# Kernel tuning notes

Measured on AMD Instinct MI355X. Metric: run time of the kernel, lower is better.

Reference implementation:

```python
import jax, jax.numpy as jnp
import numpy as np

EPS = 1e-5  # BatchNorm eps; BN applied in eval mode with running_mean=0, running_var=1


def conv1x1(x, w, b=None):
    # x: [B,C,H,W], w: [O,C] -> [B,O,H,W]
    y = jnp.einsum('bchw,oc->bohw', x, w)
    if b is not None:
        y = y + b[None, :, None, None]
    return y


def bn_eval(x, gamma, beta):
    # running_mean=0, running_var=1
    scale = gamma / jnp.sqrt(1.0 + EPS)
    return x * scale[None, :, None, None] + beta[None, :, None, None]


def glnl_forward(x, mask, wt_nl, bt_nl, wp_nl, bp_nl, wt_l, bt_l, wp_l, bp_l,
                 wg_nl, bg_nl, wg_l, bg_l, wW, bW, gW, betaW, wWl, gWl, betaWl):
    B, C, H, W = x.shape
    I = wt_nl.shape[0]
    N = H * W

    # non-local branch score [B,N,N]
    th_nl = conv1x1(x, wt_nl, bt_nl).reshape(B, I, N)
    ph_nl = conv1x1(x, wp_nl, bp_nl).reshape(B, I, N)
    score_nl = jax.nn.softmax(jnp.einsum('bin,bim->bnm', th_nl, ph_nl), axis=-1)

    # local branch: mask-gated projections, score [B,N,N]
    m = mask.reshape(B, 1, N)
    th_l = conv1x1(x, wt_l, bt_l).reshape(B, I, N) * m
    ph_l = conv1x1(x, wp_l, bp_l).reshape(B, I, N) * m
    score_l = jax.nn.softmax(jnp.einsum('bin,bim->bnm', th_l, ph_l), axis=-1)

    # value projections [B,I,N]
    g_nl = conv1x1(x, wg_nl, bg_nl).reshape(B, I, N)
    g_l = conv1x1(x, wg_l, bg_l).reshape(B, I, N)

    # attention aggregation -> [B,I,H,W]
    y_nl = jnp.einsum('bnm,bim->bin', score_nl, g_nl).reshape(B, I, H, W)
    y_l = jnp.einsum('bnm,bim->bin', score_l, g_l).reshape(B, I, H, W)

    # W_local: conv1x1 (no bias) -> ReLU -> BN
    y_l = bn_eval(jax.nn.relu(conv1x1(y_l, wWl)), gWl, betaWl)

    y = y_nl + y_l
    # W: conv1x1 -> ReLU -> BN, then residual
    W_y = bn_eval(jax.nn.relu(conv1x1(y, wW, bW)), gW, betaW)
    return W_y + x


def setup_inputs() -> dict:
    key = jax.random.key(0)
    ks = jax.random.split(key, 20)
    B, C, I, H, W = 4, 128, 64, 64, 64
    s = 0.02
    inp = {
        'x': jax.random.normal(ks[0], (B, C, H, W), jnp.float32),
        'mask': (jax.random.uniform(ks[1], (B, 1, H, W)) > 0.5).astype(jnp.float32),
        'wt_nl': jax.random.normal(ks[2], (I, C)) * s, 'bt_nl': jnp.zeros((I,)),
        'wp_nl': jax.random.normal(ks[3], (I, C)) * s, 'bp_nl': jnp.zeros((I,)),
        'wt_l': jax.random.normal(ks[4], (I, C)) * s, 'bt_l': jnp.zeros((I,)),
        'wp_l': jax.random.normal(ks[5], (I, C)) * s, 'bp_l': jnp.zeros((I,)),
        'wg_nl': jax.random.normal(ks[6], (I, C)) * s, 'bg_nl': jnp.zeros((I,)),
        'wg_l': jax.random.normal(ks[7], (I, C)) * s, 'bg_l': jnp.zeros((I,)),
        'wW': jax.random.normal(ks[8], (C, I)) * s, 'bW': jnp.zeros((C,)),
        'gW': jnp.ones((C,)), 'betaW': jnp.zeros((C,)),
        'wWl': jax.random.normal(ks[9], (I, I)) * s,
        'gWl': jnp.ones((I,)), 'betaWl': jnp.zeros((I,)),
    }
    return inp


def reference(x, mask, wt_nl, bt_nl, wp_nl, bp_nl, wt_l, bt_l, wp_l, bp_l,
              wg_nl, bg_nl, wg_l, bg_l, wW, bW, gW, betaW, wWl, gWl, betaWl):
    return glnl_forward(x, mask, wt_nl, bt_nl, wp_nl, bp_nl, wt_l, bt_l, wp_l, bp_l,
                        wg_nl, bg_nl, wg_l, bg_l, wW, bW, gW, betaW, wWl, gWl, betaWl)
```

## Files before the change

### kernel.cpp

```cpp
#include <hip/hip_runtime.h>

typedef unsigned short u16;
typedef __attribute__((ext_vector_type(8))) short short8;
typedef __attribute__((ext_vector_type(4))) float floatx4;

#define MFMA16(a, b, c) __builtin_amdgcn_mfma_f32_16x16x32_bf16((a), (b), (c), 0, 0, 0)

#define SZ_P ((size_t)4 * 64 * 4096)
#define SZ_X ((size_t)4 * 128 * 4096)

__device__ __forceinline__ float bf2f(u16 u) {
    union { unsigned int i; float f; } v; v.i = ((unsigned int)u) << 16; return v.f;
}
__device__ __forceinline__ u16 f2bf(float f) {
    union { float f; unsigned int i; } v; v.f = f;
    unsigned int r = v.i + 0x7fffu + ((v.i >> 16) & 1u);
    return (u16)(r >> 16);
}
__device__ __forceinline__ unsigned int pk2(float a, float b) {
    union { float f; unsigned int u; } x, y; x.f = a; y.f = b;
    return (x.u >> 16) | (y.u & 0xffff0000u);
}

__global__ __launch_bounds__(256) void k_prep_x(const float* __restrict__ x,
                                                u16* __restrict__ xT) {
    __shared__ u16 tile[64][65];
    const int n0 = blockIdx.x * 64, c0 = blockIdx.y * 64, b = blockIdx.z;
    const int t = threadIdx.x;
    for (int idx = t; idx < 4096; idx += 256) {
        const int c = idx >> 6, n = idx & 63;
        tile[c][n] = f2bf(x[((size_t)b << 19) + ((size_t)(c0 + c) << 12) + n0 + n]);
    }
    __syncthreads();
    for (int idx = t; idx < 4096; idx += 256) {
        const int n = idx >> 6, c = idx & 63;
        xT[((size_t)b << 19) + (size_t)(n0 + n) * 128 + c0 + c] = tile[c][n];
    }
}

__global__ __launch_bounds__(256) void k_prep_w(
    const float* __restrict__ w0, const float* __restrict__ w1,
    const float* __restrict__ w2, const float* __restrict__ w3,
    const float* __restrict__ w4, const float* __restrict__ w5,
    const float* __restrict__ wWl, const float* __restrict__ wW,
    u16* __restrict__ wbf)
{
    const int idx = blockIdx.x * 256 + threadIdx.x;
    float v;
    if (idx < 49152) {
        const int j = idx >> 13, off = idx & 8191;
        const float* s = (j == 0) ? w0 : (j == 1) ? w1 : (j == 2) ? w2
                       : (j == 3) ? w3 : (j == 4) ? w4 : w5;
        v = s[off];
    } else if (idx < 53248) {
        v = wWl[idx - 49152];
    } else {
        v = wW[idx - 53248];
    }
    wbf[idx] = f2bf(v);
}

__global__ __launch_bounds__(256) void k_proj(
    const u16* __restrict__ xT, const float* __restrict__ mask,
    const u16* __restrict__ wbf,
    const float* __restrict__ bq0f, const float* __restrict__ bk0f,
    const float* __restrict__ bv0f,
    const float* __restrict__ bq1f, const float* __restrict__ bk1f,
    const float* __restrict__ bv1f,
    u16* __restrict__ q0, u16* __restrict__ k0, u16* __restrict__ v0,
    u16* __restrict__ q1, u16* __restrict__ k1, u16* __restrict__ v1)
{
    const int n0 = blockIdx.x * 64, b = blockIdx.y, br = blockIdx.z;
    const u16* wq = wbf + br * 24576;
    const u16* wk = wq + 8192;
    const u16* wv = wk + 8192;
    const float* bq = br ? bq1f : bq0f;
    const float* bk = br ? bk1f : bk0f;
    const float* bv = br ? bv1f : bv0f;
    u16* q = br ? q1 : q0;  u16* k = br ? k1 : k0;  u16* v = br ? v1 : v0;

    const int t = threadIdx.x, w = t >> 6, lane = t & 63;
    const int quad = lane >> 4, l15 = lane & 15;
    const u16* xb = xT + ((size_t)b << 19) + (size_t)n0 * 128;

    short8 ax[4];
#pragma unroll
    for (int cc = 0; cc < 4; ++cc)
        ax[cc] = *(const short8*)(xb + (w * 16 + l15) * 128 + quad * 8 + cc * 32);

    float mv[4] = {1.f, 1.f, 1.f, 1.f};
    if (br) {
#pragma unroll
        for (int r = 0; r < 4; ++r)
            mv[r] = mask[((size_t)b << 12) + n0 + w * 16 + quad * 4 + r];
    }

#pragma unroll
    for (int qk = 0; qk < 2; ++qk) {
        const u16* wsel = qk ? wk : wq;
        const float* bb = qk ? bk : bq;
        u16* o = qk ? k : q;
#pragma unroll
        for (int ns = 0; ns < 4; ++ns) {
            floatx4 acc = {0.f, 0.f, 0.f, 0.f};
            const u16* wp = wsel + (ns * 16 + l15) * 128 + quad * 8;
#pragma unroll
            for (int cc = 0; cc < 4; ++cc)
                acc = MFMA16(ax[cc], *(const short8*)(wp + cc * 32), acc);
            const float bias_i = bb[ns * 16 + l15];
#pragma unroll
            for (int r = 0; r < 4; ++r) {
                const float val = (acc[r] + bias_i) * mv[r];
                o[((size_t)b << 18) + (size_t)(n0 + w * 16 + quad * 4 + r) * 64
                  + ns * 16 + l15] = f2bf(val);
            }
        }
    }

    short8 aw[4];
#pragma unroll
    for (int cc = 0; cc < 4; ++cc)
        aw[cc] = *(const short8*)(wv + (w * 16 + l15) * 128 + quad * 8 + cc * 32);
    float bvr[4];
#pragma unroll
    for (int r = 0; r < 4; ++r) bvr[r] = bv[w * 16 + quad * 4 + r];
#pragma unroll
    for (int ns = 0; ns < 4; ++ns) {
        floatx4 acc = {0.f, 0.f, 0.f, 0.f};
#pragma unroll
        for (int cc = 0; cc < 4; ++cc)
            acc = MFMA16(aw[cc],
                *(const short8*)(xb + (ns * 16 + l15) * 128 + quad * 8 + cc * 32), acc);
#pragma unroll
        for (int r = 0; r < 4; ++r) {
            v[((size_t)b << 18) + ((size_t)(w * 16 + quad * 4 + r) << 12)
              + n0 + ns * 16 + l15] = f2bf(acc[r] + bvr[r]);
        }
    }
}

__global__ __launch_bounds__(256) void k_flash(
    const u16* __restrict__ Q0, const u16* __restrict__ K0,
    const u16* __restrict__ V0,
    const u16* __restrict__ Q1, const u16* __restrict__ K1,
    const u16* __restrict__ V1,
    u16* __restrict__ num, float* __restrict__ den)
{
    __shared__ __align__(16) u16 kt_s[2][64 * 72];
    __shared__ __align__(16) u16 vt_s[2][64 * 72];
    __shared__ __align__(16) u16 p_s[4 * 32 * 72];

    const int flat = blockIdx.x;
    const int g = flat & 15, tile = flat >> 4;
    const int b = g >> 2, z = g & 3;
    const int br = z >> 1, sp = z & 1;
    const int qb = tile * 128;
    const size_t base = ((size_t)b << 18);
    const u16* Q = (br ? Q1 : Q0) + base;
    const u16* K = (br ? K1 : K0) + base;
    const u16* V = (br ? V1 : V0) + base;
    u16* numo = num + (size_t)z * SZ_P + base;
    float* deno = den + z * 16384 + b * 4096;

    const int t = threadIdx.x, w = t >> 6, lane = t & 63;
    const int quad = lane >> 4, l15 = lane & 15;
    const int pw = w * 32 * 72;

    short8 aq[2][2];
#pragma unroll
    for (int t2 = 0; t2 < 2; ++t2)
#pragma unroll
        for (int s = 0; s < 2; ++s)
            aq[t2][s] = *(const short8*)(Q + (size_t)(qb + w * 32 + t2 * 16 + l15) * 64
                                         + s * 32 + quad * 8);

    floatx4 oacc[4][2];
#pragma unroll
    for (int it = 0; it < 4; ++it)
#pragma unroll
        for (int t2 = 0; t2 < 2; ++t2) oacc[it][t2] = (floatx4){0.f, 0.f, 0.f, 0.f};
    float dacc[2] = {0.f, 0.f};

    const int roff = tile & 31;
    const int m_beg = sp * 2048;

    {
        const int m0 = m_beg + (roff << 6);
#pragma unroll
        for (int u = 0; u < 2; ++u) {
            const int ch = t + u * 256, row = ch >> 3, cg = ch & 7;
            *(short8*)&kt_s[0][row * 72 + cg * 8] =
                *(const short8*)(K + (size_t)(m0 + row) * 64 + cg * 8);
            *(short8*)&vt_s[0][row * 72 + cg * 8] =
                *(const short8*)(V + ((size_t)row << 12) + m0 + cg * 8);
        }
    }

    for (int j = 0; j < 32; ++j) {
        const int cur = j & 1;
        const int mn = m_beg + (((roff + j + 1) & 31) << 6);
        short8 pkr[2], pvr[2];
#pragma unroll
        for (int u = 0; u < 2; ++u) {
            const int ch = t + u * 256, row = ch >> 3, cg = ch & 7;
            pkr[u] = *(const short8*)(K + (size_t)(mn + row) * 64 + cg * 8);
            pvr[u] = *(const short8*)(V + ((size_t)row << 12) + mn + cg * 8);
        }
        __syncthreads();

#pragma unroll
        for (int mt = 0; mt < 4; ++mt) {
            const u16* kp = &kt_s[cur][(mt * 16 + l15) * 72 + quad * 8];
            const short8 ka0 = *(const short8*)kp;
            const short8 ka1 = *(const short8*)(kp + 32);
#pragma unroll
            for (int t2 = 0; t2 < 2; ++t2) {
                floatx4 acc = {0.f, 0.f, 0.f, 0.f};
                acc = MFMA16(ka0, aq[t2][0], acc);
                acc = MFMA16(ka1, aq[t2][1], acc);
                const float e0 = __expf(acc[0]), e1 = __expf(acc[1]);
                const float e2 = __expf(acc[2]), e3 = __expf(acc[3]);
                dacc[t2] += (e0 + e1) + (e2 + e3);
                *(uint2*)&p_s[pw + (t2 * 16 + l15) * 72 + mt * 16 + quad * 4] =
                    make_uint2(pk2(e0, e1), pk2(e2, e3));
            }
        }

        short8 pb2[2][2];
#pragma unroll
        for (int t2 = 0; t2 < 2; ++t2)
#pragma unroll
            for (int s = 0; s < 2; ++s)
                pb2[t2][s] = *(const short8*)&p_s[pw + (t2 * 16 + l15) * 72 + s * 32 + quad * 8];
#pragma unroll
        for (int it = 0; it < 4; ++it) {
            const u16* vp = &vt_s[cur][(it * 16 + l15) * 72 + quad * 8];
            const short8 va0 = *(const short8*)vp;
            const short8 va1 = *(const short8*)(vp + 32);
#pragma unroll
            for (int t2 = 0; t2 < 2; ++t2) {
                oacc[it][t2] = MFMA16(va0, pb2[t2][0], oacc[it][t2]);
                oacc[it][t2] = MFMA16(va1, pb2[t2][1], oacc[it][t2]);
            }
        }

#pragma unroll
        for (int u = 0; u < 2; ++u) {
            const int ch = t + u * 256, row = ch >> 3, cg = ch & 7;
            *(short8*)&kt_s[cur ^ 1][row * 72 + cg * 8] = pkr[u];
            *(short8*)&vt_s[cur ^ 1][row * 72 + cg * 8] = pvr[u];
        }
    }

#pragma unroll
    for (int t2 = 0; t2 < 2; ++t2) {
        float d = dacc[t2];
        d += __shfl_xor(d, 16, 64);
        d += __shfl_xor(d, 32, 64);
        if (quad == 0) deno[qb + w * 32 + t2 * 16 + l15] = d;
    }

#pragma unroll
    for (int it = 0; it < 4; ++it)
#pragma unroll
        for (int t2 = 0; t2 < 2; ++t2) {
            *(uint2*)&p_s[pw + (t2 * 16 + l15) * 72 + it * 16 + quad * 4] =
                make_uint2(pk2(oacc[it][t2][0], oacc[it][t2][1]),
                           pk2(oacc[it][t2][2], oacc[it][t2][3]));
        }
    __syncthreads();
#pragma unroll
    for (int ch = t; ch < 1024; ch += 256) {
        const int row = ch >> 3, cg = ch & 7;
        *(short8*)(numo + (size_t)(qb + row) * 64 + cg * 8) =
            *(const short8*)&p_s[(row >> 5) * 2304 + (row & 31) * 72 + cg * 8];
    }
}

__global__ __launch_bounds__(256) void k_epi(
    const u16* __restrict__ num, const float* __restrict__ den,
    const u16* __restrict__ wbf,
    const float* __restrict__ gWl, const float* __restrict__ betaWl,
    const float* __restrict__ bW, const float* __restrict__ gW,
    const float* __restrict__ betaW,
    const float* __restrict__ x, float* __restrict__ out)
{
    __shared__ __align__(16) u16 yl_s[32 * 72];
    __shared__ __align__(16) u16 ynl_s[32 * 72];
    __shared__ __align__(16) u16 yy_s[32 * 72];
    const int b = blockIdx.y, n0 = blockIdx.x * 32, rb = blockIdx.z;
    const int t = threadIdx.x, w = t >> 6, lane = t & 63;
    const int quad = lane >> 4, l15 = lane & 15;
    const size_t ybase = ((size_t)b << 18) + (size_t)n0 * 64;

    {
        const int row = t >> 3, cg = t & 7;
        const float dn = den[b * 4096 + n0 + row] + den[16384 + b * 4096 + n0 + row];
        const float dl = den[32768 + b * 4096 + n0 + row] + den[49152 + b * 4096 + n0 + row];
        const float inl = 1.0f / dn, ilo = 1.0f / dl;
        const short8 a0 = *(const short8*)(num + ybase + row * 64 + cg * 8);
        const short8 a1 = *(const short8*)(num + SZ_P + ybase + row * 64 + cg * 8);
        const short8 c0 = *(const short8*)(num + 2 * SZ_P + ybase + row * 64 + cg * 8);
        const short8 c1 = *(const short8*)(num + 3 * SZ_P + ybase + row * 64 + cg * 8);
        short8 ynl8, yl8;
#pragma unroll
        for (int j = 0; j < 8; ++j) {
            ynl8[j] = (short)f2bf((bf2f((u16)a0[j]) + bf2f((u16)a1[j])) * inl);
            yl8[j]  = (short)f2bf((bf2f((u16)c0[j]) + bf2f((u16)c1[j])) * ilo);
        }
        *(short8*)&ynl_s[row * 72 + cg * 8] = ynl8;
        *(short8*)&yl_s[row * 72 + cg * 8] = yl8;
    }
    __syncthreads();
    const float rsq = rsqrtf(1.0f + 1e-5f);
    const u16* wblW = wbf + 49152;
    const u16* wbW  = wbf + 53248;

    {
        const short8 a0 = *(const short8*)(wblW + (w * 16 + l15) * 64 + quad * 8);
        const short8 a1 = *(const short8*)(wblW + (w * 16 + l15) * 64 + 32 + quad * 8);
        float sc[4], bt[4];
#pragma unroll
        for (int r = 0; r < 4; ++r) {
            const int io = w * 16 + quad * 4 + r;
            sc[r] = gWl[io] * rsq;
            bt[r] = betaWl[io];
        }
#pragma unroll
        for (int ns = 0; ns < 2; ++ns) {
            floatx4 acc = {0.f, 0.f, 0.f, 0.f};
            const u16* bp_ = &yl_s[(ns * 16 + l15) * 72 + quad * 8];
            acc = MFMA16(a0, *(const short8*)bp_, acc);
            acc = MFMA16(a1, *(const short8*)(bp_ + 32), acc);
#pragma unroll
            for (int r = 0; r < 4; ++r) {
                const int io = w * 16 + quad * 4 + r;
                float val = fmaxf(acc[r], 0.f) * sc[r] + bt[r];
                val += bf2f(ynl_s[(ns * 16 + l15) * 72 + io]);
                yy_s[(ns * 16 + l15) * 72 + io] = f2bf(val);
            }
        }
    }
    __syncthreads();

    {
        const int c0 = rb * 64 + w * 16;
        const short8 a0 = *(const short8*)(wbW + (c0 + l15) * 64 + quad * 8);
        const short8 a1 = *(const short8*)(wbW + (c0 + l15) * 64 + 32 + quad * 8);
        float bs[4], sc[4], bt[4];
#pragma unroll
        for (int r = 0; r < 4; ++r) {
            const int c = c0 + quad * 4 + r;
            bs[r] = bW[c];
            sc[r] = gW[c] * rsq;
            bt[r] = betaW[c];
        }
#pragma unroll
        for (int ns = 0; ns < 2; ++ns) {
            floatx4 acc = {0.f, 0.f, 0.f, 0.f};
            const u16* bp_ = &yy_s[(ns * 16 + l15) * 72 + quad * 8];
            acc = MFMA16(a0, *(const short8*)bp_, acc);
            acc = MFMA16(a1, *(const short8*)(bp_ + 32), acc);
#pragma unroll
            for (int r = 0; r < 4; ++r) {
                const int c = c0 + quad * 4 + r;
                float val = fmaxf(acc[r] + bs[r], 0.f) * sc[r] + bt[r];
                const size_t xi = ((size_t)b << 19) + ((size_t)c << 12) + n0 + ns * 16 + l15;
                out[xi] = val + x[xi];
            }
        }
    }
}

extern "C" void kernel_launch(void* const* d_in, const int* in_sizes, int n_in,
                              void* d_out, int out_size, void* d_ws, size_t ws_size,
                              hipStream_t stream) {
    const float* x      = (const float*)d_in[0];
    const float* mask   = (const float*)d_in[1];
    const float* wt_nl  = (const float*)d_in[2];  const float* bt_nl = (const float*)d_in[3];
    const float* wp_nl  = (const float*)d_in[4];  const float* bp_nl = (const float*)d_in[5];
    const float* wt_l   = (const float*)d_in[6];  const float* bt_l  = (const float*)d_in[7];
    const float* wp_l   = (const float*)d_in[8];  const float* bp_l  = (const float*)d_in[9];
    const float* wg_nl  = (const float*)d_in[10]; const float* bg_nl = (const float*)d_in[11];
    const float* wg_l   = (const float*)d_in[12]; const float* bg_l  = (const float*)d_in[13];
    const float* wW     = (const float*)d_in[14]; const float* bW    = (const float*)d_in[15];
    const float* gW     = (const float*)d_in[16]; const float* betaW = (const float*)d_in[17];
    const float* wWl    = (const float*)d_in[18]; const float* gWl   = (const float*)d_in[19];
    const float* betaWl = (const float*)d_in[20];

    u16* ws  = (u16*)d_ws;
    u16* xT  = ws;
    u16* wbf = xT + SZ_X;
    u16* q0  = wbf + 61440;
    u16* k0  = q0 + SZ_P;
    u16* v0  = k0 + SZ_P;
    u16* q1  = v0 + SZ_P;
    u16* k1  = q1 + SZ_P;
    u16* v1  = k1 + SZ_P;
    u16* num = v1 + SZ_P;
    float* den = (float*)(num + 4 * SZ_P);

    k_prep_x<<<dim3(64, 2, 4), 256, 0, stream>>>(x, xT);
    k_prep_w<<<dim3(240), 256, 0, stream>>>(wt_nl, wp_nl, wg_nl,
                                            wt_l, wp_l, wg_l, wWl, wW, wbf);
    k_proj<<<dim3(64, 4, 2), 256, 0, stream>>>(xT, mask, wbf,
        bt_nl, bp_nl, bg_nl, bt_l, bp_l, bg_l,
        q0, k0, v0, q1, k1, v1);
    k_flash<<<dim3(512), 256, 0, stream>>>(q0, k0, v0, q1, k1, v1, num, den);
    k_epi<<<dim3(128, 4, 2), 256, 0, stream>>>(num, den, wbf, gWl, betaWl,
                                               bW, gW, betaW, x, (float*)d_out);
}
```

Before: 185.4 us.

## Fuse x transpose into projection, MFMA row sums, retile epilogue

Removes the separate x-to-bf16 transpose kernel: the projection kernel now loads fp32 x directly, converts it and transposes it in shared memory, and splits its output columns across twice as many blocks. In the flash kernel, the softmax denominator is now accumulated with an MFMA against a vector of ones instead of scalar adds plus a shuffle reduction, and K/V load addresses are precomputed outside the loop. The epilogue now uses 16-column tiles, with each block covering all output channels instead of splitting them across blocks. The fused path re-reads and re-transposes x in every projection block and adds MFMA work per tile.

```diff
diff --git a/kernel.cpp b/kernel.cpp
--- a/kernel.cpp
+++ b/kernel.cpp
@@ -7,7 +7,6 @@
 #define MFMA16(a, b, c) __builtin_amdgcn_mfma_f32_16x16x32_bf16((a), (b), (c), 0, 0, 0)
 
 #define SZ_P ((size_t)4 * 64 * 4096)
-#define SZ_X ((size_t)4 * 128 * 4096)
 
 __device__ __forceinline__ float bf2f(u16 u) {
     union { unsigned int i; float f; } v; v.i = ((unsigned int)u) << 16; return v.f;
@@ -20,22 +19,6 @@
 __device__ __forceinline__ unsigned int pk2(float a, float b) {
     union { float f; unsigned int u; } x, y; x.f = a; y.f = b;
     return (x.u >> 16) | (y.u & 0xffff0000u);
-}
-
-__global__ __launch_bounds__(256) void k_prep_x(const float* __restrict__ x,
-                                                u16* __restrict__ xT) {
-    __shared__ u16 tile[64][65];
-    const int n0 = blockIdx.x * 64, c0 = blockIdx.y * 64, b = blockIdx.z;
-    const int t = threadIdx.x;
-    for (int idx = t; idx < 4096; idx += 256) {
-        const int c = idx >> 6, n = idx & 63;
-        tile[c][n] = f2bf(x[((size_t)b << 19) + ((size_t)(c0 + c) << 12) + n0 + n]);
-    }
-    __syncthreads();
-    for (int idx = t; idx < 4096; idx += 256) {
-        const int n = idx >> 6, c = idx & 63;
-        xT[((size_t)b << 19) + (size_t)(n0 + n) * 128 + c0 + c] = tile[c][n];
-    }
 }
 
 __global__ __launch_bounds__(256) void k_prep_w(
@@ -61,7 +44,7 @@
 }
 
 __global__ __launch_bounds__(256) void k_proj(
-    const u16* __restrict__ xT, const float* __restrict__ mask,
+    const float* __restrict__ x, const float* __restrict__ mask,
     const u16* __restrict__ wbf,
     const float* __restrict__ bq0f, const float* __restrict__ bk0f,
     const float* __restrict__ bv0f,
@@ -70,7 +53,9 @@
     u16* __restrict__ q0, u16* __restrict__ k0, u16* __restrict__ v0,
     u16* __restrict__ q1, u16* __restrict__ k1, u16* __restrict__ v1)
 {
-    const int n0 = blockIdx.x * 64, b = blockIdx.y, br = blockIdx.z;
+    __shared__ __align__(16) u16 xt_s[64 * 136];
+    const int n0 = blockIdx.x * 64, b = blockIdx.y;
+    const int br = blockIdx.z >> 1, half = blockIdx.z & 1;
     const u16* wq = wbf + br * 24576;
     const u16* wk = wq + 8192;
     const u16* wv = wk + 8192;
@@ -81,12 +66,18 @@
 
     const int t = threadIdx.x, w = t >> 6, lane = t & 63;
     const int quad = lane >> 4, l15 = lane & 15;
-    const u16* xb = xT + ((size_t)b << 19) + (size_t)n0 * 128;
+    const float* xb = x + ((size_t)b << 19);
+
+    for (int idx = t; idx < 8192; idx += 256) {
+        const int c = idx >> 6, n = idx & 63;
+        xt_s[n * 136 + c] = f2bf(xb[((size_t)c << 12) + n0 + n]);
+    }
+    __syncthreads();
 
     short8 ax[4];
 #pragma unroll
     for (int cc = 0; cc < 4; ++cc)
-        ax[cc] = *(const short8*)(xb + (w * 16 + l15) * 128 + quad * 8 + cc * 32);
+        ax[cc] = *(const short8*)&xt_s[(w * 16 + l15) * 136 + quad * 8 + cc * 32];
 
     float mv[4] = {1.f, 1.f, 1.f, 1.f};
     if (br) {
@@ -101,7 +92,8 @@
         const float* bb = qk ? bk : bq;
         u16* o = qk ? k : q;
 #pragma unroll
-        for (int ns = 0; ns < 4; ++ns) {
+        for (int nsh = 0; nsh < 2; ++nsh) {
+            const int ns = half * 2 + nsh;
             floatx4 acc = {0.f, 0.f, 0.f, 0.f};
             const u16* wp = wsel + (ns * 16 + l15) * 128 + quad * 8;
 #pragma unroll
@@ -125,12 +117,13 @@
 #pragma unroll
     for (int r = 0; r < 4; ++r) bvr[r] = bv[w * 16 + quad * 4 + r];
 #pragma unroll
-    for (int ns = 0; ns < 4; ++ns) {
+    for (int nsh = 0; nsh < 2; ++nsh) {
+        const int ns = half * 2 + nsh;
         floatx4 acc = {0.f, 0.f, 0.f, 0.f};
 #pragma unroll
         for (int cc = 0; cc < 4; ++cc)
             acc = MFMA16(aw[cc],
-                *(const short8*)(xb + (ns * 16 + l15) * 128 + quad * 8 + cc * 32), acc);
+                *(const short8*)&xt_s[(ns * 16 + l15) * 136 + quad * 8 + cc * 32], acc);
 #pragma unroll
         for (int r = 0; r < 4; ++r) {
             v[((size_t)b << 18) + ((size_t)(w * 16 + quad * 4 + r) << 12)
@@ -166,6 +159,13 @@
     const int quad = lane >> 4, l15 = lane & 15;
     const int pw = w * 32 * 72;
 
+    const int r0 = t >> 3, r1 = (t + 256) >> 3, cg8 = (t & 7) * 8;
+    const u16* Kp0 = K + (size_t)r0 * 64 + cg8;
+    const u16* Kp1 = K + (size_t)r1 * 64 + cg8;
+    const u16* Vp0 = V + ((size_t)r0 << 12) + cg8;
+    const u16* Vp1 = V + ((size_t)r1 << 12) + cg8;
+    const int lk0 = r0 * 72 + cg8, lk1 = r1 * 72 + cg8;
+
     short8 aq[2][2];
 #pragma unroll
     for (int t2 = 0; t2 < 2; ++t2)
@@ -174,38 +174,33 @@
             aq[t2][s] = *(const short8*)(Q + (size_t)(qb + w * 32 + t2 * 16 + l15) * 64
                                          + s * 32 + quad * 8);
 
+    const short8 ones8 = {0x3F80, 0x3F80, 0x3F80, 0x3F80, 0x3F80, 0x3F80, 0x3F80, 0x3F80};
+
     floatx4 oacc[4][2];
 #pragma unroll
     for (int it = 0; it < 4; ++it)
 #pragma unroll
         for (int t2 = 0; t2 < 2; ++t2) oacc[it][t2] = (floatx4){0.f, 0.f, 0.f, 0.f};
-    float dacc[2] = {0.f, 0.f};
+    floatx4 lacc[2] = {{0.f, 0.f, 0.f, 0.f}, {0.f, 0.f, 0.f, 0.f}};
 
     const int roff = tile & 31;
     const int m_beg = sp * 2048;
 
     {
         const int m0 = m_beg + (roff << 6);
-#pragma unroll
-        for (int u = 0; u < 2; ++u) {
-            const int ch = t + u * 256, row = ch >> 3, cg = ch & 7;
-            *(short8*)&kt_s[0][row * 72 + cg * 8] =
-                *(const short8*)(K + (size_t)(m0 + row) * 64 + cg * 8);
-            *(short8*)&vt_s[0][row * 72 + cg * 8] =
-                *(const short8*)(V + ((size_t)row << 12) + m0 + cg * 8);
-        }
+        *(short8*)&kt_s[0][lk0] = *(const short8*)(Kp0 + (size_t)m0 * 64);
+        *(short8*)&kt_s[0][lk1] = *(const short8*)(Kp1 + (size_t)m0 * 64);
+        *(short8*)&vt_s[0][lk0] = *(const short8*)(Vp0 + m0);
+        *(short8*)&vt_s[0][lk1] = *(const short8*)(Vp1 + m0);
     }
 
     for (int j = 0; j < 32; ++j) {
         const int cur = j & 1;
         const int mn = m_beg + (((roff + j + 1) & 31) << 6);
-        short8 pkr[2], pvr[2];
-#pragma unroll
-        for (int u = 0; u < 2; ++u) {
-            const int ch = t + u * 256, row = ch >> 3, cg = ch & 7;
-            pkr[u] = *(const short8*)(K + (size_t)(mn + row) * 64 + cg * 8);
-            pvr[u] = *(const short8*)(V + ((size_t)row << 12) + mn + cg * 8);
-        }
+        short8 pk0v = *(const short8*)(Kp0 + (size_t)mn * 64);
+        short8 pk1v = *(const short8*)(Kp1 + (size_t)mn * 64);
+        short8 pv0v = *(const short8*)(Vp0 + mn);
+        short8 pv1v = *(const short8*)(Vp1 + mn);
         __syncthreads();
 
 #pragma unroll
@@ -220,7 +215,6 @@
                 acc = MFMA16(ka1, aq[t2][1], acc);
                 const float e0 = __expf(acc[0]), e1 = __expf(acc[1]);
                 const float e2 = __expf(acc[2]), e3 = __expf(acc[3]);
-                dacc[t2] += (e0 + e1) + (e2 + e3);
                 *(uint2*)&p_s[pw + (t2 * 16 + l15) * 72 + mt * 16 + quad * 4] =
                     make_uint2(pk2(e0, e1), pk2(e2, e3));
             }
@@ -243,21 +237,22 @@
                 oacc[it][t2] = MFMA16(va1, pb2[t2][1], oacc[it][t2]);
             }
         }
-
-#pragma unroll
-        for (int u = 0; u < 2; ++u) {
-            const int ch = t + u * 256, row = ch >> 3, cg = ch & 7;
-            *(short8*)&kt_s[cur ^ 1][row * 72 + cg * 8] = pkr[u];
-            *(short8*)&vt_s[cur ^ 1][row * 72 + cg * 8] = pvr[u];
-        }
-    }
-
-#pragma unroll
-    for (int t2 = 0; t2 < 2; ++t2) {
-        float d = dacc[t2];
-        d += __shfl_xor(d, 16, 64);
-        d += __shfl_xor(d, 32, 64);
-        if (quad == 0) deno[qb + w * 32 + t2 * 16 + l15] = d;
+#pragma unroll
+        for (int t2 = 0; t2 < 2; ++t2) {
+            lacc[t2] = MFMA16(ones8, pb2[t2][0], lacc[t2]);
+            lacc[t2] = MFMA16(ones8, pb2[t2][1], lacc[t2]);
+        }
+
+        *(short8*)&kt_s[cur ^ 1][lk0] = pk0v;
+        *(short8*)&kt_s[cur ^ 1][lk1] = pk1v;
+        *(short8*)&vt_s[cur ^ 1][lk0] = pv0v;
+        *(short8*)&vt_s[cur ^ 1][lk1] = pv1v;
+    }
+
+    if (quad == 0) {
+#pragma unroll
+        for (int t2 = 0; t2 < 2; ++t2)
+            deno[qb + w * 32 + t2 * 16 + l15] = lacc[t2][0];
     }
 
 #pragma unroll
@@ -285,15 +280,15 @@
     const float* __restrict__ betaW,
     const float* __restrict__ x, float* __restrict__ out)
 {
-    __shared__ __align__(16) u16 yl_s[32 * 72];
-    __shared__ __align__(16) u16 ynl_s[32 * 72];
-    __shared__ __align__(16) u16 yy_s[32 * 72];
-    const int b = blockIdx.y, n0 = blockIdx.x * 32, rb = blockIdx.z;
+    __shared__ __align__(16) u16 yl_s[16 * 72];
+    __shared__ __align__(16) u16 ynl_s[16 * 72];
+    __shared__ __align__(16) u16 yy_s[16 * 72];
+    const int b = blockIdx.y, n0 = blockIdx.x * 16;
     const int t = threadIdx.x, w = t >> 6, lane = t & 63;
     const int quad = lane >> 4, l15 = lane & 15;
     const size_t ybase = ((size_t)b << 18) + (size_t)n0 * 64;
 
-    {
+    if (t < 128) {
         const int row = t >> 3, cg = t & 7;
         const float dn = den[b * 4096 + n0 + row] + den[16384 + b * 4096 + n0 + row];
         const float dl = den[32768 + b * 4096 + n0 + row] + den[49152 + b * 4096 + n0 + row];
@@ -326,24 +321,22 @@
             sc[r] = gWl[io] * rsq;
             bt[r] = betaWl[io];
         }
-#pragma unroll
-        for (int ns = 0; ns < 2; ++ns) {
-            floatx4 acc = {0.f, 0.f, 0.f, 0.f};
-            const u16* bp_ = &yl_s[(ns * 16 + l15) * 72 + quad * 8];
-            acc = MFMA16(a0, *(const short8*)bp_, acc);
-            acc = MFMA16(a1, *(const short8*)(bp_ + 32), acc);
-#pragma unroll
-            for (int r = 0; r < 4; ++r) {
-                const int io = w * 16 + quad * 4 + r;
-                float val = fmaxf(acc[r], 0.f) * sc[r] + bt[r];
-                val += bf2f(ynl_s[(ns * 16 + l15) * 72 + io]);
-                yy_s[(ns * 16 + l15) * 72 + io] = f2bf(val);
-            }
+        floatx4 acc = {0.f, 0.f, 0.f, 0.f};
+        const u16* bp_ = &yl_s[l15 * 72 + quad * 8];
+        acc = MFMA16(a0, *(const short8*)bp_, acc);
+        acc = MFMA16(a1, *(const short8*)(bp_ + 32), acc);
+#pragma unroll
+        for (int r = 0; r < 4; ++r) {
+            const int io = w * 16 + quad * 4 + r;
+            float val = fmaxf(acc[r], 0.f) * sc[r] + bt[r];
+            val += bf2f(ynl_s[l15 * 72 + io]);
+            yy_s[l15 * 72 + io] = f2bf(val);
         }
     }
     __syncthreads();
 
-    {
+#pragma unroll
+    for (int rb = 0; rb < 2; ++rb) {
         const int c0 = rb * 64 + w * 16;
         const short8 a0 = *(const short8*)(wbW + (c0 + l15) * 64 + quad * 8);
         const short8 a1 = *(const short8*)(wbW + (c0 + l15) * 64 + 32 + quad * 8);
@@ -355,19 +348,16 @@
             sc[r] = gW[c] * rsq;
             bt[r] = betaW[c];
         }
-#pragma unroll
-        for (int ns = 0; ns < 2; ++ns) {
-            floatx4 acc = {0.f, 0.f, 0.f, 0.f};
-            const u16* bp_ = &yy_s[(ns * 16 + l15) * 72 + quad * 8];
-            acc = MFMA16(a0, *(const short8*)bp_, acc);
-            acc = MFMA16(a1, *(const short8*)(bp_ + 32), acc);
-#pragma unroll
-            for (int r = 0; r < 4; ++r) {
-                const int c = c0 + quad * 4 + r;
-                float val = fmaxf(acc[r] + bs[r], 0.f) * sc[r] + bt[r];
-                const size_t xi = ((size_t)b << 19) + ((size_t)c << 12) + n0 + ns * 16 + l15;
-                out[xi] = val + x[xi];
-            }
+        floatx4 acc = {0.f, 0.f, 0.f, 0.f};
+        const u16* bp_ = &yy_s[l15 * 72 + quad * 8];
+        acc = MFMA16(a0, *(const short8*)bp_, acc);
+        acc = MFMA16(a1, *(const short8*)(bp_ + 32), acc);
+#pragma unroll
+        for (int r = 0; r < 4; ++r) {
+            const int c = c0 + quad * 4 + r;
+            float val = fmaxf(acc[r] + bs[r], 0.f) * sc[r] + bt[r];
+            const size_t xi = ((size_t)b << 19) + ((size_t)c << 12) + n0 + l15;
+            out[xi] = val + x[xi];
         }
     }
 }
@@ -389,8 +379,7 @@
     const float* betaWl = (const float*)d_in[20];
 
     u16* ws  = (u16*)d_ws;
-    u16* xT  = ws;
-    u16* wbf = xT + SZ_X;
+    u16* wbf = ws;
     u16* q0  = wbf + 61440;
     u16* k0  = q0 + SZ_P;
     u16* v0  = k0 + SZ_P;
@@ -400,13 +389,12 @@
     u16* num = v1 + SZ_P;
     float* den = (float*)(num + 4 * SZ_P);
 
-    k_prep_x<<<dim3(64, 2, 4), 256, 0, stream>>>(x, xT);
     k_prep_w<<<dim3(240), 256, 0, stream>>>(wt_nl, wp_nl, wg_nl,
                                             wt_l, wp_l, wg_l, wWl, wW, wbf);
-    k_proj<<<dim3(64, 4, 2), 256, 0, stream>>>(xT, mask, wbf,
+    k_proj<<<dim3(64, 4, 4), 256, 0, stream>>>(x, mask, wbf,
         bt_nl, bp_nl, bg_nl, bt_l, bp_l, bg_l,
         q0, k0, v0, q1, k1, v1);
     k_flash<<<dim3(512), 256, 0, stream>>>(q0, k0, v0, q1, k1, v1, num, den);
-    k_epi<<<dim3(128, 4, 2), 256, 0, stream>>>(num, den, wbf, gWl, betaWl,
-                                               bW, gW, betaW, x, (float*)d_out);
-}
+    k_epi<<<dim3(256, 4), 256, 0, stream>>>(num, den, wbf, gWl, betaWl,
+                                            bW, gW, betaW, x, (float*)d_out);
+}
```

After: 180.6 us. 1.03x faster.
